# Performance work log

Measured on AMD Instinct MI355X. Metric: run time of the kernel, lower is better.

The kernel has to match this reference:

```python
import jax, jax.numpy as jnp
import numpy as np

EPS = 1e-12

def _normalize(v):
    # matches F.normalize(..., eps): v / max(||v||, eps)
    return v / jnp.maximum(jnp.linalg.norm(v), EPS)

def sn_weight(W, u):
    """One power iteration (num_svs=1, num_itrs=1, eval mode: u not updated).
    W: [out, in] (1x1 conv flattened). u: [1, out].
    u, v are no-grad in torch; sv = v @ W.T @ u'.T carries grad w.r.t. W."""
    v = jax.lax.stop_gradient(_normalize(jax.lax.stop_gradient(u) @ W))          # [1, in]
    u2 = jax.lax.stop_gradient(_normalize(v @ W.T))                              # [1, out]
    sv = (v @ W.T @ u2.T)[0, 0]
    return W / sv

def maxpool2x2(x):
    B, C, H, W = x.shape
    return x.reshape(B, C, H // 2, 2, W // 2, 2).max(axis=(3, 5))

def conv1x1(W, x):
    # W: [out_c, in_c], x: [B, in_c, H, W]
    return jnp.einsum('oc,bchw->bohw', W, x)

def setup_inputs() -> dict:
    key = jax.random.key(0)
    ks = jax.random.split(key, 9)
    ch = 128
    B, H, W = 16, 64, 64
    x = jax.random.normal(ks[0], (B, ch, H, W), dtype=jnp.float32)
    # 1x1 conv weights flattened to [out, in], kaiming-ish scale
    def w(k, o, i):
        return jax.random.normal(k, (o, i), dtype=jnp.float32) * (1.0 / np.sqrt(i))
    w_theta = w(ks[1], ch // 8, ch)
    w_phi   = w(ks[2], ch // 8, ch)
    w_g     = w(ks[3], ch // 2, ch)
    w_o     = w(ks[4], ch, ch // 2)
    u_theta = jax.random.normal(ks[5], (1, ch // 8), dtype=jnp.float32)
    u_phi   = jax.random.normal(ks[6], (1, ch // 8), dtype=jnp.float32)
    u_g     = jax.random.normal(ks[7], (1, ch // 2), dtype=jnp.float32)
    u_o     = jax.random.normal(ks[8], (1, ch), dtype=jnp.float32)
    gamma = jnp.float32(0.7)  # param (init 0.0 in torch; nonzero for a meaningful test)
    return dict(x=x, w_theta=w_theta, w_phi=w_phi, w_g=w_g, w_o=w_o,
                u_theta=u_theta, u_phi=u_phi, u_g=u_g, u_o=u_o, gamma=gamma)

def reference(x, w_theta, w_phi, w_g, w_o, u_theta, u_phi, u_g, u_o, gamma):
    B, C, H, W = x.shape
    Wt = sn_weight(w_theta, u_theta)
    Wp = sn_weight(w_phi, u_phi)
    Wg = sn_weight(w_g, u_g)
    Wo = sn_weight(w_o, u_o)
    theta = conv1x1(Wt, x).reshape(B, C // 8, H * W)               # [B, C/8, HW]
    phi = maxpool2x2(conv1x1(Wp, x)).reshape(B, C // 8, H * W // 4)  # [B, C/8, HW/4]
    g = maxpool2x2(conv1x1(Wg, x)).reshape(B, C // 2, H * W // 4)    # [B, C/2, HW/4]
    beta = jax.nn.softmax(jnp.einsum('bcs,bct->bst', theta, phi), axis=-1)  # [B, HW, HW/4]
    o = jnp.einsum('bct,bst->bcs', g, beta).reshape(B, C // 2, H, W)
    return gamma * conv1x1(Wo, o) + x
```

## Files before the change

kernel.cpp:

```cpp
#include <hip/hip_runtime.h>
#include <hip/hip_bf16.h>


#define U_WN  0
#define U_WO  12288
#define U_TH  20480
#define U_PHI 1069056
#define U_G   1331200
#define U_OT  2379776

typedef __attribute__((ext_vector_type(8))) short bf16x8;
typedef __attribute__((ext_vector_type(4))) short s16x4;
typedef __attribute__((ext_vector_type(4))) float f32x4;
typedef __attribute__((ext_vector_type(16))) float f32x16;

__device__ inline unsigned short f2b(float f) {
    union { float f; unsigned u; } v; v.f = f;
    unsigned r = v.u + 0x7FFFu + ((v.u >> 16) & 1u);
    return (unsigned short)(r >> 16);
}
__device__ inline float b2f(unsigned short u) {
    union { unsigned u; float f; } v; v.u = ((unsigned)u) << 16; return v.f;
}

__device__ inline unsigned cvtpk_bf16(float lo, float hi) {
    unsigned r;
    asm("s_nop 0\n\tv_cvt_pk_bf16_f32 %0, %1, %2" : "=v"(r) : "v"(lo), "v"(hi));
    return r;
}
__device__ inline void pl32swap(unsigned &a, unsigned &b) {
    asm("s_nop 1\n\tv_permlane32_swap_b32 %0, %1\n\ts_nop 1" : "+v"(a), "+v"(b));
}

__global__ __launch_bounds__(256) void sn4(
        const float* __restrict__ w0, const float* __restrict__ w1,
        const float* __restrict__ w2, const float* __restrict__ w3,
        const float* __restrict__ u0, const float* __restrict__ u1,
        const float* __restrict__ u2, const float* __restrict__ u3,
        unsigned short* __restrict__ wsu) {
    int wi = blockIdx.x;
    const float* W; const float* u; unsigned short* dst; int on, in_;
    if      (wi == 0) { W = w0; u = u0; dst = wsu;          on = 16;  in_ = 128; }
    else if (wi == 1) { W = w1; u = u1; dst = wsu + 2048;   on = 16;  in_ = 128; }
    else if (wi == 2) { W = w2; u = u2; dst = wsu + 4096;   on = 64;  in_ = 128; }
    else              { W = w3; u = u3; dst = wsu + 12288;  on = 128; in_ = 64;  }
    __shared__ float Wl[8320];
    __shared__ float ul[128];
    __shared__ float v[128];
    __shared__ float red[256];
    __shared__ float s_inv;
    int tid = threadIdx.x;
    int n = on * in_;
    int stride = in_ + 1;
    int shift = (in_ == 128) ? 7 : 6;
    int mask = in_ - 1;
    for (int i = tid; i < n; i += 256) {
        int o = i >> shift, j = i & mask;
        Wl[o * stride + j] = W[i];
    }
    if (tid < on) ul[tid] = u[tid];
    __syncthreads();
    float vi = 0.f;
    if (tid < in_) {
        for (int o = 0; o < on; ++o) vi += ul[o] * Wl[o * stride + tid];
    }
    red[tid] = (tid < in_) ? vi * vi : 0.f;
    __syncthreads();
    for (int st = 128; st > 0; st >>= 1) {
        if (tid < st) red[tid] += red[tid + st];
        __syncthreads();
    }
    float inv_nv = 1.0f / fmaxf(sqrtf(red[0]), 1e-12f);
    __syncthreads();
    if (tid < in_) v[tid] = vi * inv_nv;
    __syncthreads();
    float ui = 0.f;
    if (tid < on) {
        for (int i = 0; i < in_; ++i) ui += v[i] * Wl[tid * stride + i];
    }
    red[tid] = (tid < on) ? ui * ui : 0.f;
    __syncthreads();
    for (int st = 128; st > 0; st >>= 1) {
        if (tid < st) red[tid] += red[tid + st];
        __syncthreads();
    }
    if (tid == 0) {
        float nsq = red[0];
        float sv = nsq / fmaxf(sqrtf(nsq), 1e-12f);
        s_inv = 1.0f / sv;
    }
    __syncthreads();
    float inv = s_inv;
    for (int e = tid; e < n; e += 256) {
        int o = e >> shift, j = e & mask;
        dst[e] = f2b(Wl[o * stride + j] * inv);
    }
}

__global__ __launch_bounds__(512, 4) void convpool_mfma(
        const float* __restrict__ x, const unsigned short* __restrict__ wn,
        unsigned short* __restrict__ thetaT, unsigned short* __restrict__ phiT,
        unsigned short* __restrict__ gT) {
    __shared__ unsigned short xT[128 * 136];
    __shared__ unsigned short wnl[96 * 136];
    int tid = threadIdx.x;
    int bb = blockIdx.x >> 5, tile = blockIdx.x & 31;
    int px0 = tile << 7;
    for (int i = tid; i < 1536; i += 512) {
        int r = i >> 4, c8 = (i & 15) * 8;
        *(bf16x8*)&wnl[r * 136 + c8] = *(const bf16x8*)&wn[r * 128 + c8];
    }
    const float4* x4 = (const float4*)x;
    {
        int p4 = tid & 31, cg = (tid >> 5) * 4;
        for (int k = 0; k < 2; ++k) {
            int cb = k * 64 + cg;
            float4 v0 = x4[(bb * 128 + cb + 0) * 1024 + tile * 32 + p4];
            float4 v1 = x4[(bb * 128 + cb + 1) * 1024 + tile * 32 + p4];
            float4 v2 = x4[(bb * 128 + cb + 2) * 1024 + tile * 32 + p4];
            float4 v3 = x4[(bb * 128 + cb + 3) * 1024 + tile * 32 + p4];
            float a0[4] = {v0.x, v0.y, v0.z, v0.w};
            float a1[4] = {v1.x, v1.y, v1.z, v1.w};
            float a2[4] = {v2.x, v2.y, v2.z, v2.w};
            float a3[4] = {v3.x, v3.y, v3.z, v3.w};
#pragma unroll
            for (int j = 0; j < 4; ++j) {
                union { unsigned w[2]; s16x4 v; } pk;
                pk.w[0] = cvtpk_bf16(a0[j], a1[j]);
                pk.w[1] = cvtpk_bf16(a2[j], a3[j]);
                *(s16x4*)&xT[(p4 * 4 + j) * 136 + cb] = pk.v;
            }
        }
    }
    __syncthreads();
    int lane = tid & 63, wv = tid >> 6;
    int q = lane >> 4, l = lane & 15;
    int pxw = wv * 16;
    f32x4 acc[6];
    const f32x4 z4 = {0.f, 0.f, 0.f, 0.f};
#pragma unroll
    for (int nt = 0; nt < 6; ++nt) acc[nt] = z4;
#pragma unroll
    for (int kk = 0; kk < 4; ++kk) {
        bf16x8 a0 = *(const bf16x8*)&xT[(pxw + l) * 136 + kk * 32 + q * 8];
#pragma unroll
        for (int nt = 0; nt < 6; ++nt) {
            bf16x8 bw = *(const bf16x8*)&wnl[(nt * 16 + l) * 136 + kk * 32 + q * 8];
            acc[nt] = __builtin_amdgcn_mfma_f32_16x16x32_bf16(a0, bw, acc[nt], 0, 0, 0);
        }
    }
#pragma unroll
    for (int r = 0; r < 4; ++r) {
        int s = px0 + pxw + q * 4 + r;
        thetaT[(bb * 4096 + s) * 16 + l] = f2b(acc[0][r]);
    }
    __syncthreads();
    unsigned short* poolbuf = wnl;
#pragma unroll
    for (int nt = 1; nt < 6; ++nt) {
        int ch = nt * 16 + l - 16;
#pragma unroll
        for (int r = 0; r < 4; ++r) {
            poolbuf[ch * 132 + pxw + q * 4 + r] = f2b(acc[nt][r]);
        }
    }
    __syncthreads();
    for (int i = tid; i < 2560; i += 512) {
        int tcol = i & 31, ch = i >> 5;
        int base = ch * 132 + tcol * 2;
        float m0 = fmaxf(b2f(poolbuf[base]), b2f(poolbuf[base + 1]));
        float m1 = fmaxf(b2f(poolbuf[base + 64]), b2f(poolbuf[base + 65]));
        float m = fmaxf(m0, m1);
        int t = tile * 32 + tcol;
        if (ch < 16) phiT[(bb * 1024 + t) * 16 + ch] = f2b(m);
        else         gT[(bb * 64 + ch - 16) * 1024 + t] = f2b(m);
    }
}

__global__ __launch_bounds__(512, 4) void attn_mfma(
        const unsigned short* __restrict__ thetaT,
        const unsigned short* __restrict__ phiT,
        const unsigned short* __restrict__ gT,
        unsigned short* __restrict__ oT) {
    __shared__ float ldsO[4][2048];
    __shared__ float ldsD[4][32];
    int tid = threadIdx.x;
    int kblk = blockIdx.x;
    int vblk = (kblk & 7) * 64 + (kblk >> 3);
    int bb = vblk >> 5, st = vblk & 31;
    int s0 = st << 7;
    int lane = tid & 63, wv = tid >> 6;
    int sg = wv & 3, sp = wv >> 2;
    int sl = lane & 31, hi = lane >> 5;
    int srow = bb * 4096 + s0 + sg * 32 + sl;
    const unsigned short* phiB = phiT + bb * 16384;
    const unsigned short* gB   = gT + bb * 65536;
    int tbase = sp << 9;

    bf16x8 bth = *(const bf16x8*)&thetaT[srow * 16 + hi * 8];

    f32x16 z16;
#pragma unroll
    for (int i = 0; i < 16; ++i) z16[i] = 0.f;
    f32x16 acc0 = z16, acc1 = z16;
    float lp4[4] = {0.f, 0.f, 0.f, 0.f};

    bf16x8 ph0 = *(const bf16x8*)&phiB[(tbase + sl) * 16 + hi * 8];
    bf16x8 ph1 = *(const bf16x8*)&phiB[(tbase + 32 + sl) * 16 + hi * 8];

    for (int tc = 0; tc < 8; ++tc) {
        int t0 = tbase + (tc << 6);
        bf16x8 gf0[4], gf1[4];
#pragma unroll
        for (int kt = 0; kt < 2; ++kt) {
            gf0[kt] = *(const bf16x8*)&gB[(sl) * 1024 + t0 + kt * 16 + hi * 8];
            gf1[kt] = *(const bf16x8*)&gB[(32 + sl) * 1024 + t0 + kt * 16 + hi * 8];
        }
        f32x16 sa = __builtin_amdgcn_mfma_f32_32x32x16_bf16(ph0, bth, z16, 0, 0, 0);
        unsigned u0[8], u1[8];
#pragma unroll
        for (int i = 0; i < 8; ++i) {
            float e0 = __expf(sa[2 * i]);
            float e1 = __expf(sa[2 * i + 1]);
            lp4[0] += e0; lp4[1] += e1;
            u0[i] = cvtpk_bf16(e0, e1);
        }
        __builtin_amdgcn_sched_barrier(0);
        f32x16 sb = __builtin_amdgcn_mfma_f32_32x32x16_bf16(ph1, bth, z16, 0, 0, 0);
        pl32swap(u0[0], u0[2]); pl32swap(u0[1], u0[3]);
        pl32swap(u0[4], u0[6]); pl32swap(u0[5], u0[7]);
#pragma unroll
        for (int kt = 2; kt < 4; ++kt) {
            gf0[kt] = *(const bf16x8*)&gB[(sl) * 1024 + t0 + kt * 16 + hi * 8];
            gf1[kt] = *(const bf16x8*)&gB[(32 + sl) * 1024 + t0 + kt * 16 + hi * 8];
        }
        int t0n = tbase + (((tc + 1) & 7) << 6);
        ph0 = *(const bf16x8*)&phiB[(t0n + sl) * 16 + hi * 8];
        ph1 = *(const bf16x8*)&phiB[(t0n + 32 + sl) * 16 + hi * 8];
#pragma unroll
        for (int i = 0; i < 8; ++i) {
            float e2 = __expf(sb[2 * i]);
            float e3 = __expf(sb[2 * i + 1]);
            lp4[2] += e2; lp4[3] += e3;
            u1[i] = cvtpk_bf16(e2, e3);
        }
        pl32swap(u1[0], u1[2]); pl32swap(u1[1], u1[3]);
        pl32swap(u1[4], u1[6]); pl32swap(u1[5], u1[7]);
        __builtin_amdgcn_s_setprio(1);
        {
            union { unsigned w[4]; bf16x8 v; } pf = {{u0[0], u0[1], u0[2], u0[3]}};
            acc0 = __builtin_amdgcn_mfma_f32_32x32x16_bf16(gf0[0], pf.v, acc0, 0, 0, 0);
            acc1 = __builtin_amdgcn_mfma_f32_32x32x16_bf16(gf1[0], pf.v, acc1, 0, 0, 0);
        }
        {
            union { unsigned w[4]; bf16x8 v; } pf = {{u0[4], u0[5], u0[6], u0[7]}};
            acc0 = __builtin_amdgcn_mfma_f32_32x32x16_bf16(gf0[1], pf.v, acc0, 0, 0, 0);
            acc1 = __builtin_amdgcn_mfma_f32_32x32x16_bf16(gf1[1], pf.v, acc1, 0, 0, 0);
        }
        {
            union { unsigned w[4]; bf16x8 v; } pf = {{u1[0], u1[1], u1[2], u1[3]}};
            acc0 = __builtin_amdgcn_mfma_f32_32x32x16_bf16(gf0[2], pf.v, acc0, 0, 0, 0);
            acc1 = __builtin_amdgcn_mfma_f32_32x32x16_bf16(gf1[2], pf.v, acc1, 0, 0, 0);
        }
        {
            union { unsigned w[4]; bf16x8 v; } pf = {{u1[4], u1[5], u1[6], u1[7]}};
            acc0 = __builtin_amdgcn_mfma_f32_32x32x16_bf16(gf0[3], pf.v, acc0, 0, 0, 0);
            acc1 = __builtin_amdgcn_mfma_f32_32x32x16_bf16(gf1[3], pf.v, acc1, 0, 0, 0);
        }
        __builtin_amdgcn_s_setprio(0);
    }
    float tot = (lp4[0] + lp4[1]) + (lp4[2] + lp4[3]);
    tot += __shfl_xor(tot, 32);

    if (sp == 1) {
#pragma unroll
        for (int i = 0; i < 16; ++i) {
            int c = (i & 3) + 8 * (i >> 2) + 4 * hi;
            ldsO[sg][c * 32 + sl] = acc0[i];
            ldsO[sg][(32 + c) * 32 + sl] = acc1[i];
        }
        if (hi == 0) ldsD[sg][sl] = tot;
    }
    __syncthreads();
    if (sp == 1) return;
    tot += ldsD[sg][sl];
    float inv = 1.0f / tot;
#pragma unroll
    for (int i = 0; i < 16; ++i) {
        int c = (i & 3) + 8 * (i >> 2) + 4 * hi;
        acc0[i] += ldsO[sg][c * 32 + sl];
        acc1[i] += ldsO[sg][(32 + c) * 32 + sl];
    }
    unsigned o0[8], o1[8];
#pragma unroll
    for (int i = 0; i < 8; ++i) {
        o0[i] = cvtpk_bf16(acc0[2 * i] * inv, acc0[2 * i + 1] * inv);
        o1[i] = cvtpk_bf16(acc1[2 * i] * inv, acc1[2 * i + 1] * inv);
    }
    pl32swap(o0[0], o0[2]); pl32swap(o0[1], o0[3]);
    pl32swap(o0[4], o0[6]); pl32swap(o0[5], o0[7]);
    pl32swap(o1[0], o1[2]); pl32swap(o1[1], o1[3]);
    pl32swap(o1[4], o1[6]); pl32swap(o1[5], o1[7]);
    unsigned short* orow = oT + srow * 64;
    {
        union { unsigned w[4]; bf16x8 v; } ow = {{o0[0], o0[1], o0[2], o0[3]}};
        *(bf16x8*)&orow[hi * 8] = ow.v;
    }
    {
        union { unsigned w[4]; bf16x8 v; } ow = {{o0[4], o0[5], o0[6], o0[7]}};
        *(bf16x8*)&orow[16 + hi * 8] = ow.v;
    }
    {
        union { unsigned w[4]; bf16x8 v; } ow = {{o1[0], o1[1], o1[2], o1[3]}};
        *(bf16x8*)&orow[32 + hi * 8] = ow.v;
    }
    {
        union { unsigned w[4]; bf16x8 v; } ow = {{o1[4], o1[5], o1[6], o1[7]}};
        *(bf16x8*)&orow[48 + hi * 8] = ow.v;
    }
}

__global__ __launch_bounds__(256, 4) void outconv_mfma(
        const unsigned short* __restrict__ oT, const unsigned short* __restrict__ wo,
        const float* __restrict__ x, const float* __restrict__ gam,
        float* __restrict__ out) {
    __shared__ unsigned short wol[128 * 72];
    int tid = threadIdx.x;
    int bb = blockIdx.x >> 6, tile = blockIdx.x & 63;
    int lane = tid & 63, wv = tid >> 6;
    int q = lane >> 4, l = lane & 15;
    int pxw = tile * 64 + wv * 16;
    for (int i = tid; i < 1024; i += 256) {
        int r = i >> 3, c8 = (i & 7) * 8;
        *(bf16x8*)&wol[r * 72 + c8] = *(const bf16x8*)&wo[r * 64 + c8];
    }
    bf16x8 af[2];
#pragma unroll
    for (int kk = 0; kk < 2; ++kk)
        af[kk] = *(const bf16x8*)&oT[(bb * 4096 + pxw + l) * 64 + kk * 32 + q * 8];
    __syncthreads();
    f32x4 acc[8];
    const f32x4 z4 = {0.f, 0.f, 0.f, 0.f};
#pragma unroll
    for (int nt = 0; nt < 8; ++nt) acc[nt] = z4;
#pragma unroll
    for (int kk = 0; kk < 2; ++kk) {
#pragma unroll
        for (int nt = 0; nt < 8; ++nt) {
            bf16x8 bw = *(const bf16x8*)&wol[(nt * 16 + l) * 72 + kk * 32 + q * 8];
            acc[nt] = __builtin_amdgcn_mfma_f32_16x16x32_bf16(af[kk], bw, acc[nt], 0, 0, 0);
        }
    }
    float gm = gam[0];
    const float4* x4 = (const float4*)x;
    float4* out4 = (float4*)out;
#pragma unroll
    for (int nt = 0; nt < 8; ++nt) {
        int oc = nt * 16 + l;
        int px = pxw + q * 4;
        int gi = (bb * 128 + oc) * 1024 + (px >> 2);
        float4 xv = x4[gi];
        float4 r;
        r.x = gm * acc[nt][0] + xv.x;
        r.y = gm * acc[nt][1] + xv.y;
        r.z = gm * acc[nt][2] + xv.z;
        r.w = gm * acc[nt][3] + xv.w;
        out4[gi] = r;
    }
}

extern "C" void kernel_launch(void* const* d_in, const int* in_sizes, int n_in,
                              void* d_out, int out_size, void* d_ws, size_t ws_size,
                              hipStream_t stream) {
    const float* x  = (const float*)d_in[0];
    const float* wt = (const float*)d_in[1];
    const float* wp = (const float*)d_in[2];
    const float* wg = (const float*)d_in[3];
    const float* wo = (const float*)d_in[4];
    const float* ut = (const float*)d_in[5];
    const float* up = (const float*)d_in[6];
    const float* ug = (const float*)d_in[7];
    const float* uo = (const float*)d_in[8];
    const float* gm = (const float*)d_in[9];
    unsigned short* wsu = (unsigned short*)d_ws;
    float* out = (float*)d_out;

    sn4<<<4, 256, 0, stream>>>(wt, wp, wg, wo, ut, up, ug, uo, wsu);
    convpool_mfma<<<512, 512, 0, stream>>>(x, wsu + U_WN,
                                           wsu + U_TH, wsu + U_PHI, wsu + U_G);
    attn_mfma<<<512, 512, 0, stream>>>(wsu + U_TH, wsu + U_PHI, wsu + U_G, wsu + U_OT);
    outconv_mfma<<<1024, 256, 0, stream>>>(wsu + U_OT, wsu + U_WO, x, gm, out);
}
```

Measured before the change: 154.3 us.

## Fuse output 1x1 conv and residual into attention kernel epilogue

Merges the attention kernel and the separate output-conv kernel. Blocks shrink to 4 waves covering 64 query rows, and the two key-half waves exchange partial sums through LDS. Each wave then applies the Wo projection to its 64-channel half with MFMA and writes gamma*conv + x directly. This removes the bf16 intermediate o round trip through global memory and one kernel launch. The cost is half as many query rows per block, so phi and g are loaded twice as often, and the new epilogue stores are scalar fp32 writes.

```diff
diff --git a/kernel.cpp b/kernel.cpp
--- a/kernel.cpp
+++ b/kernel.cpp
@@ -7,7 +7,6 @@
 #define U_TH  20480
 #define U_PHI 1069056
 #define U_G   1331200
-#define U_OT  2379776
 
 typedef __attribute__((ext_vector_type(8))) short bf16x8;
 typedef __attribute__((ext_vector_type(4))) short s16x4;
@@ -177,20 +176,22 @@
     }
 }
 
-__global__ __launch_bounds__(512, 4) void attn_mfma(
+__global__ __launch_bounds__(256, 3) void attn_out(
         const unsigned short* __restrict__ thetaT,
         const unsigned short* __restrict__ phiT,
         const unsigned short* __restrict__ gT,
-        unsigned short* __restrict__ oT) {
-    __shared__ float ldsO[4][2048];
-    __shared__ float ldsD[4][32];
+        const unsigned short* __restrict__ wo,
+        const float* __restrict__ x, const float* __restrict__ gam,
+        float* __restrict__ out) {
+    __shared__ float ldsO[2][2][2048];
+    __shared__ float ldsD[2][2][32];
     int tid = threadIdx.x;
     int kblk = blockIdx.x;
-    int vblk = (kblk & 7) * 64 + (kblk >> 3);
-    int bb = vblk >> 5, st = vblk & 31;
-    int s0 = st << 7;
+    int vblk = (kblk & 7) * 128 + (kblk >> 3);
+    int bb = vblk >> 6, st = vblk & 63;
+    int s0 = st << 6;
     int lane = tid & 63, wv = tid >> 6;
-    int sg = wv & 3, sp = wv >> 2;
+    int sg = wv & 1, sp = wv >> 1;
     int sl = lane & 31, hi = lane >> 5;
     int srow = bb * 4096 + s0 + sg * 32 + sl;
     const unsigned short* phiB = phiT + bb * 16384;
@@ -272,24 +273,28 @@
     float tot = (lp4[0] + lp4[1]) + (lp4[2] + lp4[3]);
     tot += __shfl_xor(tot, 32);
 
-    if (sp == 1) {
-#pragma unroll
-        for (int i = 0; i < 16; ++i) {
-            int c = (i & 3) + 8 * (i >> 2) + 4 * hi;
-            ldsO[sg][c * 32 + sl] = acc0[i];
-            ldsO[sg][(32 + c) * 32 + sl] = acc1[i];
-        }
-        if (hi == 0) ldsD[sg][sl] = tot;
-    }
-    __syncthreads();
-    if (sp == 1) return;
-    tot += ldsD[sg][sl];
-    float inv = 1.0f / tot;
 #pragma unroll
     for (int i = 0; i < 16; ++i) {
         int c = (i & 3) + 8 * (i >> 2) + 4 * hi;
-        acc0[i] += ldsO[sg][c * 32 + sl];
-        acc1[i] += ldsO[sg][(32 + c) * 32 + sl];
+        ldsO[sg][sp][c * 32 + sl] = acc0[i];
+        ldsO[sg][sp][(32 + c) * 32 + sl] = acc1[i];
+    }
+    if (hi == 0) ldsD[sg][sp][sl] = tot;
+    bf16x8 aw[2][4];
+#pragma unroll
+    for (int mt = 0; mt < 2; ++mt)
+#pragma unroll
+        for (int ch = 0; ch < 4; ++ch)
+            aw[mt][ch] = *(const bf16x8*)&wo[(sp * 64 + mt * 32 + sl) * 64 + ch * 16 + hi * 8];
+    __syncthreads();
+    int osp = sp ^ 1;
+    tot += ldsD[sg][osp][sl];
+    float inv = 1.0f / tot;
+#pragma unroll
+    for (int i = 0; i < 16; ++i) {
+        int c = (i & 3) + 8 * (i >> 2) + 4 * hi;
+        acc0[i] += ldsO[sg][osp][c * 32 + sl];
+        acc1[i] += ldsO[sg][osp][(32 + c) * 32 + sl];
     }
     unsigned o0[8], o1[8];
 #pragma unroll
@@ -301,71 +306,29 @@
     pl32swap(o0[4], o0[6]); pl32swap(o0[5], o0[7]);
     pl32swap(o1[0], o1[2]); pl32swap(o1[1], o1[3]);
     pl32swap(o1[4], o1[6]); pl32swap(o1[5], o1[7]);
-    unsigned short* orow = oT + srow * 64;
+    bf16x8 bfr[4];
     {
-        union { unsigned w[4]; bf16x8 v; } ow = {{o0[0], o0[1], o0[2], o0[3]}};
-        *(bf16x8*)&orow[hi * 8] = ow.v;
-    }
-    {
-        union { unsigned w[4]; bf16x8 v; } ow = {{o0[4], o0[5], o0[6], o0[7]}};
-        *(bf16x8*)&orow[16 + hi * 8] = ow.v;
-    }
-    {
-        union { unsigned w[4]; bf16x8 v; } ow = {{o1[0], o1[1], o1[2], o1[3]}};
-        *(bf16x8*)&orow[32 + hi * 8] = ow.v;
-    }
-    {
-        union { unsigned w[4]; bf16x8 v; } ow = {{o1[4], o1[5], o1[6], o1[7]}};
-        *(bf16x8*)&orow[48 + hi * 8] = ow.v;
-    }
-}
-
-__global__ __launch_bounds__(256, 4) void outconv_mfma(
-        const unsigned short* __restrict__ oT, const unsigned short* __restrict__ wo,
-        const float* __restrict__ x, const float* __restrict__ gam,
-        float* __restrict__ out) {
-    __shared__ unsigned short wol[128 * 72];
-    int tid = threadIdx.x;
-    int bb = blockIdx.x >> 6, tile = blockIdx.x & 63;
-    int lane = tid & 63, wv = tid >> 6;
-    int q = lane >> 4, l = lane & 15;
-    int pxw = tile * 64 + wv * 16;
-    for (int i = tid; i < 1024; i += 256) {
-        int r = i >> 3, c8 = (i & 7) * 8;
-        *(bf16x8*)&wol[r * 72 + c8] = *(const bf16x8*)&wo[r * 64 + c8];
-    }
-    bf16x8 af[2];
-#pragma unroll
-    for (int kk = 0; kk < 2; ++kk)
-        af[kk] = *(const bf16x8*)&oT[(bb * 4096 + pxw + l) * 64 + kk * 32 + q * 8];
-    __syncthreads();
-    f32x4 acc[8];
-    const f32x4 z4 = {0.f, 0.f, 0.f, 0.f};
-#pragma unroll
-    for (int nt = 0; nt < 8; ++nt) acc[nt] = z4;
-#pragma unroll
-    for (int kk = 0; kk < 2; ++kk) {
-#pragma unroll
-        for (int nt = 0; nt < 8; ++nt) {
-            bf16x8 bw = *(const bf16x8*)&wol[(nt * 16 + l) * 72 + kk * 32 + q * 8];
-            acc[nt] = __builtin_amdgcn_mfma_f32_16x16x32_bf16(af[kk], bw, acc[nt], 0, 0, 0);
-        }
+        union { unsigned w[4]; bf16x8 v; } t;
+        t.w[0] = o0[0]; t.w[1] = o0[1]; t.w[2] = o0[2]; t.w[3] = o0[3]; bfr[0] = t.v;
+        t.w[0] = o0[4]; t.w[1] = o0[5]; t.w[2] = o0[6]; t.w[3] = o0[7]; bfr[1] = t.v;
+        t.w[0] = o1[0]; t.w[1] = o1[1]; t.w[2] = o1[2]; t.w[3] = o1[3]; bfr[2] = t.v;
+        t.w[0] = o1[4]; t.w[1] = o1[5]; t.w[2] = o1[6]; t.w[3] = o1[7]; bfr[3] = t.v;
+    }
+    f32x16 d0 = z16, d1 = z16;
+#pragma unroll
+    for (int ch = 0; ch < 4; ++ch) {
+        d0 = __builtin_amdgcn_mfma_f32_32x32x16_bf16(aw[0][ch], bfr[ch], d0, 0, 0, 0);
+        d1 = __builtin_amdgcn_mfma_f32_32x32x16_bf16(aw[1][ch], bfr[ch], d1, 0, 0, 0);
     }
     float gm = gam[0];
-    const float4* x4 = (const float4*)x;
-    float4* out4 = (float4*)out;
-#pragma unroll
-    for (int nt = 0; nt < 8; ++nt) {
-        int oc = nt * 16 + l;
-        int px = pxw + q * 4;
-        int gi = (bb * 128 + oc) * 1024 + (px >> 2);
-        float4 xv = x4[gi];
-        float4 r;
-        r.x = gm * acc[nt][0] + xv.x;
-        r.y = gm * acc[nt][1] + xv.y;
-        r.z = gm * acc[nt][2] + xv.z;
-        r.w = gm * acc[nt][3] + xv.w;
-        out4[gi] = r;
+    int scol = s0 + sg * 32 + sl;
+#pragma unroll
+    for (int i = 0; i < 16; ++i) {
+        int r = (i & 3) + 8 * (i >> 2) + 4 * hi;
+        int a0 = (bb * 128 + sp * 64 + r) * 4096 + scol;
+        int a1 = (bb * 128 + sp * 64 + 32 + r) * 4096 + scol;
+        out[a0] = gm * d0[i] + x[a0];
+        out[a1] = gm * d1[i] + x[a1];
     }
 }
 
@@ -388,6 +351,6 @@
     sn4<<<4, 256, 0, stream>>>(wt, wp, wg, wo, ut, up, ug, uo, wsu);
     convpool_mfma<<<512, 512, 0, stream>>>(x, wsu + U_WN,
                                            wsu + U_TH, wsu + U_PHI, wsu + U_G);
-    attn_mfma<<<512, 512, 0, stream>>>(wsu + U_TH, wsu + U_PHI, wsu + U_G, wsu + U_OT);
-    outconv_mfma<<<1024, 256, 0, stream>>>(wsu + U_OT, wsu + U_WO, x, gm, out);
-}
+    attn_out<<<1024, 256, 0, stream>>>(wsu + U_TH, wsu + U_PHI, wsu + U_G,
+                                       wsu + U_WO, x, gm, out);
+}
```

Result: faster. 148.1 us (-4.0%).
